# Kernel optimization log

Measured on AMD Instinct MI355X. Metric: run time of the kernel, lower is better.

Reference implementation:

```python
import jax, jax.numpy as jnp
import numpy as np

SHAPES = [(100, 100), (50, 50), (25, 25), (13, 13)]
N_HEADS, N_LEVELS, N_POINTS, D_MODEL, D_FFN = 8, 4, 4, 256, 1024
HEAD_DIM = D_MODEL // N_HEADS
S_TOTAL = sum(h * w for h, w in SHAPES)
BATCH = 2


def _layernorm(x, g, b, eps=1e-5):
    m = jnp.mean(x, -1, keepdims=True)
    v = jnp.mean((x - m) ** 2, -1, keepdims=True)
    return (x - m) * jax.lax.rsqrt(v + eps) * g + b


def _bilinear_sample(value_l, loc, Hl, Wl):
    # value_l: (N, Hl, Wl, nh, hd); loc: (N, Lq, nh, P, 2) normalized to [0,1]
    # Matches torch grid_sample(mode='bilinear', padding_mode='zeros', align_corners=False)
    x = loc[..., 0] * Wl - 0.5
    y = loc[..., 1] * Hl - 0.5
    x0 = jnp.floor(x); y0 = jnp.floor(y)
    wx1 = x - x0; wx0 = 1.0 - wx1
    wy1 = y - y0; wy0 = 1.0 - wy1
    x0i = x0.astype(jnp.int32); x1i = x0i + 1
    y0i = y0.astype(jnp.int32); y1i = y0i + 1
    N, Lq, nh, P = x.shape
    n_idx = jnp.arange(N)[:, None, None, None]
    h_idx = jnp.arange(nh)[None, None, :, None]

    def gather(yi, xi):
        valid = (yi >= 0) & (yi < Hl) & (xi >= 0) & (xi < Wl)
        yc = jnp.clip(yi, 0, Hl - 1); xc = jnp.clip(xi, 0, Wl - 1)
        v = value_l[n_idx, yc, xc, h_idx]  # (N, Lq, nh, P, hd)
        return v * valid[..., None].astype(v.dtype)

    return (gather(y0i, x0i) * (wy0 * wx0)[..., None]
            + gather(y0i, x1i) * (wy0 * wx1)[..., None]
            + gather(y1i, x0i) * (wy1 * wx0)[..., None]
            + gather(y1i, x1i) * (wy1 * wx1)[..., None])


def _forward(src, pos, reference_points, W_off, b_off, W_attn, b_attn, W_val, b_val,
             W_out, b_out, W1, b1, W2, b2, g1, beta1, g2, beta2):
    N, S, C = src.shape
    q = src + pos  # with_pos_embed
    # MSDeformAttn
    off = (q @ W_off + b_off).reshape(N, S, N_HEADS, N_LEVELS, N_POINTS, 2)
    aw = jax.nn.softmax((q @ W_attn + b_attn).reshape(N, S, N_HEADS, N_LEVELS * N_POINTS), axis=-1)
    aw = aw.reshape(N, S, N_HEADS, N_LEVELS, N_POINTS)
    value = (src @ W_val + b_val).reshape(N, S, N_HEADS, HEAD_DIM)
    # offset normalizer is (W_l, H_l) per level
    normalizer = jnp.array([[wl, hl] for hl, wl in SHAPES], dtype=src.dtype)  # (L, 2)
    loc = reference_points[:, :, None, :, None, :] + off / normalizer[None, None, None, :, None, :]
    out = jnp.zeros((N, S, N_HEADS, HEAD_DIM), src.dtype)
    start = 0
    for l, (Hl, Wl) in enumerate(SHAPES):
        v_l = value[:, start:start + Hl * Wl].reshape(N, Hl, Wl, N_HEADS, HEAD_DIM)
        sampled = _bilinear_sample(v_l, loc[:, :, :, l], Hl, Wl)  # (N,S,nh,P,hd)
        out = out + jnp.einsum('nqhp,nqhpd->nqhd', aw[:, :, :, l], sampled)
        start += Hl * Wl
    src2 = out.reshape(N, S, C) @ W_out + b_out
    # residual + norm1 (dropout is identity in eval)
    x = _layernorm(src + src2, g1, beta1)
    # FFN + residual + norm2
    ff = jax.nn.relu(x @ W1 + b1) @ W2 + b2
    return _layernorm(x + ff, g2, beta2)


def setup_inputs() -> dict:
    key = jax.random.key(0)
    ks = jax.random.split(key, 16)
    f32 = jnp.float32

    def w(k, shape, scale=0.02):
        return jax.random.normal(k, shape, dtype=f32) * scale

    return {
        "src": jax.random.normal(ks[0], (BATCH, S_TOTAL, D_MODEL), dtype=f32),
        "pos": jax.random.normal(ks[1], (BATCH, S_TOTAL, D_MODEL), dtype=f32),
        "reference_points": jax.random.uniform(ks[2], (BATCH, S_TOTAL, N_LEVELS, 2), dtype=f32),
        "spatial_shapes": jnp.array(SHAPES, dtype=jnp.int32),
        "level_start_index": jnp.array(np.cumsum([0] + [h * w for h, w in SHAPES[:-1]]), dtype=jnp.int32),
        "W_off": w(ks[3], (D_MODEL, N_HEADS * N_LEVELS * N_POINTS * 2)),
        "b_off": w(ks[4], (N_HEADS * N_LEVELS * N_POINTS * 2,), 0.5),
        "W_attn": w(ks[5], (D_MODEL, N_HEADS * N_LEVELS * N_POINTS)),
        "b_attn": w(ks[6], (N_HEADS * N_LEVELS * N_POINTS,)),
        "W_val": w(ks[7], (D_MODEL, D_MODEL)),
        "b_val": w(ks[8], (D_MODEL,)),
        "W_out": w(ks[9], (D_MODEL, D_MODEL)),
        "b_out": w(ks[10], (D_MODEL,)),
        "W1": w(ks[11], (D_MODEL, D_FFN)),
        "b1": w(ks[12], (D_FFN,)),
        "W2": w(ks[13], (D_FFN, D_MODEL)),
        "b2": w(ks[14], (D_MODEL,)),
        "g1": jnp.ones((D_MODEL,), f32),
        "beta1": jnp.zeros((D_MODEL,), f32),
        "g2": jnp.ones((D_MODEL,), f32),
        "beta2": jnp.zeros((D_MODEL,), f32),
    }


def reference(src, pos, reference_points, spatial_shapes, level_start_index,
              W_off, b_off, W_attn, b_attn, W_val, b_val, W_out, b_out,
              W1, b1, W2, b2, g1, beta1, g2, beta2):
    # spatial_shapes / level_start_index are static metadata mirrored by SHAPES
    return _forward(src, pos, reference_points, W_off, b_off, W_attn, b_attn,
                    W_val, b_val, W_out, b_out, W1, b1, W2, b2, g1, beta1, g2, beta2)
```

## Files before the change

### kernel.cpp

```cpp
#include <hip/hip_runtime.h>


typedef __bf16 bf16x8 __attribute__((ext_vector_type(8)));
typedef __bf16 bf16x4 __attribute__((ext_vector_type(4)));
typedef float floatx4 __attribute__((ext_vector_type(4)));

#define S_TOTAL 13294
#define M_ROWS  26588
#define M_PAD   26624
#define DMODEL  256

#define GLDS(g, l)                                                            \
    __builtin_amdgcn_global_load_lds(                                         \
        (const __attribute__((address_space(1))) void*)(g),                   \
        (__attribute__((address_space(3))) void*)(l), 16, 0, 0)

struct CvtArgs {
    const float *Woff, *Wattn, *Wval, *Wout, *W1, *W2, *boff, *battn;
};
__global__ __launch_bounds__(256) void cvt_all(CvtArgs a, __bf16* __restrict__ wdst,
                                               float* __restrict__ bc) {
    int i = blockIdx.x * 256 + threadIdx.x;
    if (i < 65536) {
        wdst[i] = (__bf16)a.Woff[(i & 255) * 256 + (i >> 8)];
    } else if (i < 98304) {
        int j = i - 65536;
        wdst[i] = (__bf16)a.Wattn[(j & 255) * 128 + (j >> 8)];
    } else if (i < 163840) {
        int j = i - 98304;
        wdst[i] = (__bf16)a.Wval[(j & 255) * 256 + (j >> 8)];
    } else if (i < 229376) {
        int j = i - 163840;
        wdst[i] = (__bf16)a.Wout[(j & 255) * 256 + (j >> 8)];
    } else if (i < 491520) {
        int j = i - 229376;
        wdst[i] = (__bf16)a.W1[(j & 255) * 1024 + (j >> 8)];
    } else if (i < 753664) {
        int j = i - 491520;
        wdst[i] = (__bf16)a.W2[(j & 1023) * 256 + (j >> 10)];
    } else if (i < 754048) {
        int j = i - 753664;
        bc[j] = (j < 256) ? a.boff[j] : a.battn[j - 256];
    }
}

__global__ __launch_bounds__(256) void prep_k(const float* __restrict__ src,
                                              const float* __restrict__ pos,
                                              __bf16* __restrict__ qb,
                                              __bf16* __restrict__ srcb) {
    int i4 = blockIdx.x * 256 + threadIdx.x;
    size_t e = (size_t)i4 * 4;
    if (e < (size_t)M_ROWS * DMODEL) {
        float4 s = *(const float4*)(src + e);
        float4 p = *(const float4*)(pos + e);
        bf16x4 q = {(__bf16)(s.x + p.x), (__bf16)(s.y + p.y),
                    (__bf16)(s.z + p.z), (__bf16)(s.w + p.w)};
        bf16x4 sb = {(__bf16)s.x, (__bf16)s.y, (__bf16)s.z, (__bf16)s.w};
        *(bf16x4*)(qb + e)   = q;
        *(bf16x4*)(srcb + e) = sb;
    } else {
        bf16x4 z = {(__bf16)0.f, (__bf16)0.f, (__bf16)0.f, (__bf16)0.f};
        *(bf16x4*)(qb + e)   = z;
        *(bf16x4*)(srcb + e) = z;
    }
}

template <bool RELU, bool BF16OUT, bool ACCUM>
__global__ __launch_bounds__(256, 2) void gemm128(const __bf16* __restrict__ A,
                                                  const __bf16* __restrict__ BT,
                                                  const float* __restrict__ bias,
                                                  float* __restrict__ Cf,
                                                  __bf16* __restrict__ Cb,
                                                  int N, int K, int ldb) {
    __shared__ __align__(16) char smem[20480];
    __bf16* As = (__bf16*)smem;
    __bf16* Bs = (__bf16*)(smem + 8192);
    const int tid  = threadIdx.x;
    const int bm   = blockIdx.y, bn = blockIdx.x;
    const int wave = tid >> 6, lane = tid & 63;
    const int wr   = wave >> 1, wc = wave & 1;
    const int l16  = lane & 15, quad = lane >> 4;

    floatx4 acc[4][4] = {};

    const int lr = tid >> 2;
    const int lc = (tid & 3) * 8;
    const __bf16* Ag0 = A  + (size_t)(bm * 128 + lr) * K + lc;
    const __bf16* Ag1 = Ag0 + (size_t)64 * K;
    const __bf16* Bg0 = BT + (size_t)(bn * 128 + lr) * ldb + lc;
    const __bf16* Bg1 = Bg0 + (size_t)64 * ldb;
    __bf16* Al0 = As + tid * 8;
    __bf16* Al1 = As + 64 * 32 + tid * 8;
    __bf16* Bl0 = Bs + tid * 8;
    __bf16* Bl1 = Bs + 64 * 32 + tid * 8;

    for (int k0 = 0; k0 < K; k0 += 32) {
        __syncthreads();
        GLDS(Ag0 + k0, Al0);
        GLDS(Ag1 + k0, Al1);
        GLDS(Bg0 + k0, Bl0);
        GLDS(Bg1 + k0, Bl1);
        __syncthreads();
        bf16x8 af[4], bfr[4];
#pragma unroll
        for (int i = 0; i < 4; i++)
            af[i] = *(const bf16x8*)(As + (wr * 64 + i * 16 + l16) * 32 + quad * 8);
#pragma unroll
        for (int j = 0; j < 4; j++)
            bfr[j] = *(const bf16x8*)(Bs + (wc * 64 + j * 16 + l16) * 32 + quad * 8);
#pragma unroll
        for (int i = 0; i < 4; i++)
#pragma unroll
            for (int j = 0; j < 4; j++)
                acc[i][j] = __builtin_amdgcn_mfma_f32_16x16x32_bf16(
                    af[i], bfr[j], acc[i][j], 0, 0, 0);
    }

    __syncthreads();
    float* patch = (float*)smem + wave * (64 * 20);
    const int row0 = bm * 128 + wr * 64;
    const int col0 = bn * 128 + wc * 64;
    const int plr = lane >> 2, plc = lane & 3;

#pragma unroll
    for (int j = 0; j < 4; j++) {
        int   n  = col0 + j * 16 + l16;
        float bv = bias ? bias[n] : 0.f;
#pragma unroll
        for (int i = 0; i < 4; i++)
#pragma unroll
            for (int r = 0; r < 4; r++) {
                float v = acc[i][j][r] + bv;
                if (RELU) v = fmaxf(v, 0.f);
                patch[(i * 16 + quad * 4 + r) * 20 + l16] = v;
            }
#pragma unroll
        for (int rr = 0; rr < 4; rr++) {
            int row = rr * 16 + plr;
            float4 v4 = *(float4*)&patch[row * 20 + plc * 4];
            size_t gi = (size_t)(row0 + row) * N + col0 + j * 16 + plc * 4;
            if (BF16OUT) {
                bf16x4 ob = {(__bf16)v4.x, (__bf16)v4.y, (__bf16)v4.z, (__bf16)v4.w};
                *(bf16x4*)(Cb + gi) = ob;
            } else if (ACCUM) {
                float4 c4 = *(const float4*)(Cf + gi);
                v4.x += c4.x; v4.y += c4.y; v4.z += c4.z; v4.w += c4.w;
                *(float4*)(Cf + gi) = v4;
            } else {
                *(float4*)(Cf + gi) = v4;
            }
        }
    }
}

__global__ __launch_bounds__(256) void sample_k(const float* __restrict__ offa,
                                                const __bf16* __restrict__ valb,
                                                const float* __restrict__ refp,
                                                __bf16* __restrict__ outb) {
    const int r   = blockIdx.x;
    const int tid = threadIdx.x;
    if (r >= M_ROWS) {
        outb[(size_t)r * 256 + tid] = (__bf16)0.f;
        return;
    }
    __shared__ float2 s_wo[128][4];
    const int n = (r >= S_TOTAL) ? 1 : 0;

    if (tid < 128) {
        const int HLc[4] = {100, 50, 25, 13};
        const int STc[4] = {0, 10000, 12500, 13125};
        int lp = tid & 15, l = lp >> 2;
        float logit = offa[(size_t)r * 384 + 256 + tid];
        float mx = logit;
        mx = fmaxf(mx, __shfl_xor(mx, 1));
        mx = fmaxf(mx, __shfl_xor(mx, 2));
        mx = fmaxf(mx, __shfl_xor(mx, 4));
        mx = fmaxf(mx, __shfl_xor(mx, 8));
        float e = __expf(logit - mx);
        float s = e;
        s += __shfl_xor(s, 1); s += __shfl_xor(s, 2);
        s += __shfl_xor(s, 4); s += __shfl_xor(s, 8);
        float aw = e / s;

        float2 o2 = *(const float2*)(offa + (size_t)r * 384 + tid * 2);
        float rx = refp[((size_t)r * 4 + l) * 2];
        float ry = refp[((size_t)r * 4 + l) * 2 + 1];
        int   Wl = HLc[l];
        float x = rx * (float)Wl + o2.x - 0.5f;
        float y = ry * (float)Wl + o2.y - 0.5f;
        float xf = floorf(x), yf = floorf(y);
        float wx1 = x - xf, wy1 = y - yf;
        float wx0 = 1.f - wx1, wy0 = 1.f - wy1;
        int x0 = (int)xf, y0 = (int)yf;
        int base = n * S_TOTAL + STc[l];
#pragma unroll
        for (int c = 0; c < 4; c++) {
            int yy = y0 + (c >> 1), xx = x0 + (c & 1);
            bool valid = (yy >= 0) & (yy < Wl) & (xx >= 0) & (xx < Wl);
            int yc = min(max(yy, 0), Wl - 1);
            int xc = min(max(xx, 0), Wl - 1);
            float w = ((c >> 1) ? wy1 : wy0) * ((c & 1) ? wx1 : wx0);
            int off = (base + yc * Wl + xc) * 512;
            s_wo[tid][c] = make_float2(valid ? w * aw : 0.f, __int_as_float(off));
        }
    }
    __syncthreads();

    const int h  = tid >> 5;
    const int pg = (tid >> 2) & 7;
    const int cg = tid & 3;
    const char* vbase = (const char*)valb + h * 64 + cg * 16;
    float a[8] = {};
#pragma unroll
    for (int pp = 0; pp < 2; pp++) {
        int idx = h * 16 + pg * 2 + pp;
#pragma unroll
        for (int c = 0; c < 4; c++) {
            float2 wo = s_wo[idx][c];
            float  w  = wo.x;
            bf16x8 v  = *(const bf16x8*)(vbase + __float_as_int(wo.y));
#pragma unroll
            for (int k = 0; k < 8; k++) a[k] += w * (float)v[k];
        }
    }
#pragma unroll
    for (int k = 0; k < 8; k++) {
        a[k] += __shfl_xor(a[k], 4);
        a[k] += __shfl_xor(a[k], 8);
        a[k] += __shfl_xor(a[k], 16);
    }
    if (pg == 0) {
        bf16x8 res;
#pragma unroll
        for (int k = 0; k < 8; k++) res[k] = (__bf16)a[k];
        *(bf16x8*)(outb + (size_t)r * 256 + h * 32 + cg * 8) = res;
    }
}

__global__ __launch_bounds__(64) void ln1_k(const float* __restrict__ src,
                                            const float* __restrict__ src2,
                                            const float* __restrict__ g,
                                            const float* __restrict__ b,
                                            float* __restrict__ x,
                                            __bf16* __restrict__ xb) {
    const int r = blockIdx.x, lane = threadIdx.x;
    if (r >= M_ROWS) {
        bf16x4 z = {(__bf16)0.f, (__bf16)0.f, (__bf16)0.f, (__bf16)0.f};
        *(bf16x4*)(xb + (size_t)r * 256 + lane * 4) = z;
        return;
    }
    size_t base = (size_t)r * 256 + lane * 4;
    float4 a = *(const float4*)(src + base);
    float4 c = *(const float4*)(src2 + base);
    float v0 = a.x + c.x, v1 = a.y + c.y, v2 = a.z + c.z, v3 = a.w + c.w;
    float s  = v0 + v1 + v2 + v3;
    float sq = v0 * v0 + v1 * v1 + v2 * v2 + v3 * v3;
    for (int o = 32; o > 0; o >>= 1) {
        s  += __shfl_xor(s, o);
        sq += __shfl_xor(sq, o);
    }
    float mean = s * (1.f / 256.f);
    float var  = sq * (1.f / 256.f) - mean * mean;
    float rs   = rsqrtf(var + 1e-5f);
    float4 gg = *(const float4*)(g + lane * 4);
    float4 bb = *(const float4*)(b + lane * 4);
    float o0 = (v0 - mean) * rs * gg.x + bb.x;
    float o1 = (v1 - mean) * rs * gg.y + bb.y;
    float o2 = (v2 - mean) * rs * gg.z + bb.z;
    float o3 = (v3 - mean) * rs * gg.w + bb.w;
    *(float4*)(x + base) = make_float4(o0, o1, o2, o3);
    bf16x4 ob = {(__bf16)o0, (__bf16)o1, (__bf16)o2, (__bf16)o3};
    *(bf16x4*)(xb + base) = ob;
}

__global__ __launch_bounds__(64) void ln2_k(const float* __restrict__ t,
                                            const float* __restrict__ g,
                                            const float* __restrict__ b,
                                            float* __restrict__ out) {
    const int r = blockIdx.x, lane = threadIdx.x;
    size_t base = (size_t)r * 256 + lane * 4;
    float4 a = *(const float4*)(t + base);
    float v0 = a.x, v1 = a.y, v2 = a.z, v3 = a.w;
    float s  = v0 + v1 + v2 + v3;
    float sq = v0 * v0 + v1 * v1 + v2 * v2 + v3 * v3;
    for (int o = 32; o > 0; o >>= 1) {
        s  += __shfl_xor(s, o);
        sq += __shfl_xor(sq, o);
    }
    float mean = s * (1.f / 256.f);
    float var  = sq * (1.f / 256.f) - mean * mean;
    float rs   = rsqrtf(var + 1e-5f);
    float4 gg = *(const float4*)(g + lane * 4);
    float4 bb = *(const float4*)(b + lane * 4);
    float4 o4;
    o4.x = (v0 - mean) * rs * gg.x + bb.x;
    o4.y = (v1 - mean) * rs * gg.y + bb.y;
    o4.z = (v2 - mean) * rs * gg.z + bb.z;
    o4.w = (v3 - mean) * rs * gg.w + bb.w;
    *(float4*)(out + base) = o4;
}

extern "C" void kernel_launch(void* const* d_in, const int* in_sizes, int n_in,
                              void* d_out, int out_size, void* d_ws, size_t ws_size,
                              hipStream_t stream) {
    const float* src  = (const float*)d_in[0];
    const float* pos  = (const float*)d_in[1];
    const float* refp = (const float*)d_in[2];
    const float* W_off  = (const float*)d_in[5];
    const float* b_off  = (const float*)d_in[6];
    const float* W_attn = (const float*)d_in[7];
    const float* b_attn = (const float*)d_in[8];
    const float* W_val  = (const float*)d_in[9];
    const float* b_val  = (const float*)d_in[10];
    const float* W_out  = (const float*)d_in[11];
    const float* b_out  = (const float*)d_in[12];
    const float* W1     = (const float*)d_in[13];
    const float* b1     = (const float*)d_in[14];
    const float* W2     = (const float*)d_in[15];
    const float* b2     = (const float*)d_in[16];
    const float* g1     = (const float*)d_in[17];
    const float* beta1  = (const float*)d_in[18];
    const float* g2     = (const float*)d_in[19];
    const float* beta2  = (const float*)d_in[20];
    float* out = (float*)d_out;

    const size_t RB = (size_t)M_PAD * 256 * 2;
    const size_t RF = (size_t)M_PAD * 256 * 4;
    char* ws = (char*)d_ws;
    __bf16* qb   = (__bf16*)(ws);
    __bf16* srcb = (__bf16*)(ws + RB);
    float*  offa = (float*)(ws + 2 * RB);
    __bf16* valb = (__bf16*)(ws + 2 * RB + (size_t)M_PAD * 384 * 4);
    __bf16* outb = qb;
    float*  src2 = (float*)(ws + RB);
    float*  x    = (float*)(ws + RB + RF);
    __bf16* xb   = qb;
    __bf16* hbh  = (__bf16*)(ws + 2 * RB + (size_t)M_PAD * 384 * 4);
    char*   regW = ws + 2 * RB + (size_t)M_PAD * 384 * 4 + (size_t)M_PAD * 512 * 2;

    __bf16* WTcomb = (__bf16*)regW;
    __bf16* WTval  = (__bf16*)(regW + 196608);
    __bf16* WTout  = (__bf16*)(regW + 327680);
    __bf16* WT1    = (__bf16*)(regW + 458752);
    __bf16* WT2    = (__bf16*)(regW + 983040);
    float*  bc     = (float*)(regW + 1507328);

    CvtArgs ca = {W_off, W_attn, W_val, W_out, W1, W2, b_off, b_attn};
    cvt_all<<<(754048 + 255) / 256, 256, 0, stream>>>(ca, WTcomb, bc);

    prep_k<<<M_PAD * 256 / 4 / 256, 256, 0, stream>>>(src, pos, qb, srcb);

    gemm128<false, false, false><<<dim3(3, M_PAD / 128), 256, 0, stream>>>(
        qb, WTcomb, bc, offa, nullptr, 384, 256, 256);
    gemm128<false, true, false><<<dim3(2, M_PAD / 128), 256, 0, stream>>>(
        srcb, WTval, b_val, nullptr, valb, 256, 256, 256);

    sample_k<<<M_PAD, 256, 0, stream>>>(offa, valb, refp, outb);

    gemm128<false, false, false><<<dim3(2, M_PAD / 128), 256, 0, stream>>>(
        outb, WTout, b_out, src2, nullptr, 256, 256, 256);
    ln1_k<<<M_PAD, 64, 0, stream>>>(src, src2, g1, beta1, x, xb);

    for (int half = 0; half < 2; half++) {
        gemm128<true, true, false><<<dim3(4, M_PAD / 128), 256, 0, stream>>>(
            xb, WT1 + (size_t)half * 512 * 256, b1 + half * 512, nullptr, hbh,
            512, 256, 256);
        gemm128<false, false, true><<<dim3(2, M_PAD / 128), 256, 0, stream>>>(
            hbh, WT2 + half * 512, half == 0 ? b2 : nullptr, x, nullptr,
            256, 512, 1024);
    }
    ln2_k<<<M_ROWS, 64, 0, stream>>>(x, g2, beta2, out);
}
```

Measured before the change: 345.1 us.

## Replace tiled GEMM with A-resident full-K GEMM reading B from global

Replaces the 128x128 k-loop GEMM with a kernel that loads the full-K A row panel (64 or 32 rows) into XOR-swizzled LDS once. Each of 8 waves then computes a slice of N with weights streamed directly from global/L2, with no per-k-step barriers. This removes the repeated syncthreads and the B staging through LDS, but relies on L2 caching for the small weight matrices. It also transposes the sampling kernel's shared weight/offset table to [corner][point] to change the LDS access pattern.

```diff
diff --git a/kernel.cpp b/kernel.cpp
--- a/kernel.cpp
+++ b/kernel.cpp
@@ -9,11 +9,6 @@
 #define M_ROWS  26588
 #define M_PAD   26624
 #define DMODEL  256
-
-#define GLDS(g, l)                                                            \
-    __builtin_amdgcn_global_load_lds(                                         \
-        (const __attribute__((address_space(1))) void*)(g),                   \
-        (__attribute__((address_space(3))) void*)(l), 16, 0, 0)
 
 struct CvtArgs {
     const float *Woff, *Wattn, *Wval, *Wout, *W1, *W2, *boff, *battn;
@@ -65,80 +60,76 @@
     }
 }
 
-template <bool RELU, bool BF16OUT, bool ACCUM>
-__global__ __launch_bounds__(256, 2) void gemm128(const __bf16* __restrict__ A,
-                                                  const __bf16* __restrict__ BT,
-                                                  const float* __restrict__ bias,
-                                                  float* __restrict__ Cf,
-                                                  __bf16* __restrict__ Cb,
-                                                  int N, int K, int ldb) {
-    __shared__ __align__(16) char smem[20480];
-    __bf16* As = (__bf16*)smem;
-    __bf16* Bs = (__bf16*)(smem + 8192);
+template <int BM, int KT, int J, bool RELU, bool BF16OUT, bool ACCUM>
+__global__ __launch_bounds__(512, 4) void gemm_ares(const __bf16* __restrict__ A,
+                                                    int lda,
+                                                    const __bf16* __restrict__ BT,
+                                                    int ldb,
+                                                    const float* __restrict__ bias,
+                                                    float* __restrict__ Cf,
+                                                    __bf16* __restrict__ Cb,
+                                                    int N) {
+    constexpr int GPR = KT / 8;
+    __shared__ __align__(16) __bf16 As[BM * KT];
+    __shared__ __align__(16) float  patch[8][16 * 20];
+
     const int tid  = threadIdx.x;
-    const int bm   = blockIdx.y, bn = blockIdx.x;
+    const int row0 = blockIdx.y * BM;
     const int wave = tid >> 6, lane = tid & 63;
-    const int wr   = wave >> 1, wc = wave & 1;
     const int l16  = lane & 15, quad = lane >> 4;
 
-    floatx4 acc[4][4] = {};
-
-    const int lr = tid >> 2;
-    const int lc = (tid & 3) * 8;
-    const __bf16* Ag0 = A  + (size_t)(bm * 128 + lr) * K + lc;
-    const __bf16* Ag1 = Ag0 + (size_t)64 * K;
-    const __bf16* Bg0 = BT + (size_t)(bn * 128 + lr) * ldb + lc;
-    const __bf16* Bg1 = Bg0 + (size_t)64 * ldb;
-    __bf16* Al0 = As + tid * 8;
-    __bf16* Al1 = As + 64 * 32 + tid * 8;
-    __bf16* Bl0 = Bs + tid * 8;
-    __bf16* Bl1 = Bs + 64 * 32 + tid * 8;
-
-    for (int k0 = 0; k0 < K; k0 += 32) {
-        __syncthreads();
-        GLDS(Ag0 + k0, Al0);
-        GLDS(Ag1 + k0, Al1);
-        GLDS(Bg0 + k0, Bl0);
-        GLDS(Bg1 + k0, Bl1);
-        __syncthreads();
-        bf16x8 af[4], bfr[4];
-#pragma unroll
-        for (int i = 0; i < 4; i++)
-            af[i] = *(const bf16x8*)(As + (wr * 64 + i * 16 + l16) * 32 + quad * 8);
-#pragma unroll
-        for (int j = 0; j < 4; j++)
-            bfr[j] = *(const bf16x8*)(Bs + (wc * 64 + j * 16 + l16) * 32 + quad * 8);
-#pragma unroll
-        for (int i = 0; i < 4; i++)
-#pragma unroll
-            for (int j = 0; j < 4; j++)
+#pragma unroll
+    for (int it = 0; it < BM * GPR / 512; it++) {
+        int fg = it * 512 + tid;
+        int m  = fg / GPR, g = fg % GPR;
+        bf16x8 v = *(const bf16x8*)(A + (size_t)(row0 + m) * lda + g * 8);
+        *(bf16x8*)(As + m * KT + (g ^ (m & 31)) * 8) = v;
+    }
+    __syncthreads();
+
+    const int n0 = blockIdx.x * (8 * J * 16) + wave * (J * 16);
+    floatx4 acc[BM / 16][J] = {};
+
+#pragma unroll 4
+    for (int ki = 0; ki < KT / 32; ki++) {
+        bf16x8 af[BM / 16], bfr[J];
+#pragma unroll
+        for (int i = 0; i < BM / 16; i++) {
+            int row = i * 16 + l16;
+            int g   = ki * 4 + quad;
+            af[i] = *(const bf16x8*)(As + row * KT + (g ^ (row & 31)) * 8);
+        }
+#pragma unroll
+        for (int j = 0; j < J; j++) {
+            int n = n0 + j * 16 + l16;
+            bfr[j] = *(const bf16x8*)(BT + (size_t)n * ldb + ki * 32 + quad * 8);
+        }
+#pragma unroll
+        for (int i = 0; i < BM / 16; i++)
+#pragma unroll
+            for (int j = 0; j < J; j++)
                 acc[i][j] = __builtin_amdgcn_mfma_f32_16x16x32_bf16(
                     af[i], bfr[j], acc[i][j], 0, 0, 0);
     }
 
-    __syncthreads();
-    float* patch = (float*)smem + wave * (64 * 20);
-    const int row0 = bm * 128 + wr * 64;
-    const int col0 = bn * 128 + wc * 64;
-    const int plr = lane >> 2, plc = lane & 3;
-
-#pragma unroll
-    for (int j = 0; j < 4; j++) {
-        int   n  = col0 + j * 16 + l16;
-        float bv = bias ? bias[n] : 0.f;
-#pragma unroll
-        for (int i = 0; i < 4; i++)
+    float bvj[J];
+#pragma unroll
+    for (int j = 0; j < J; j++) bvj[j] = bias ? bias[n0 + j * 16 + l16] : 0.f;
+
+    float* pat = patch[wave];
+    const int prow = lane >> 2, pc = lane & 3;
+#pragma unroll
+    for (int i = 0; i < BM / 16; i++)
+#pragma unroll
+        for (int j = 0; j < J; j++) {
 #pragma unroll
             for (int r = 0; r < 4; r++) {
-                float v = acc[i][j][r] + bv;
+                float v = acc[i][j][r] + bvj[j];
                 if (RELU) v = fmaxf(v, 0.f);
-                patch[(i * 16 + quad * 4 + r) * 20 + l16] = v;
+                pat[(quad * 4 + r) * 20 + l16] = v;
             }
-#pragma unroll
-        for (int rr = 0; rr < 4; rr++) {
-            int row = rr * 16 + plr;
-            float4 v4 = *(float4*)&patch[row * 20 + plc * 4];
-            size_t gi = (size_t)(row0 + row) * N + col0 + j * 16 + plc * 4;
+            float4 v4 = *(float4*)&pat[prow * 20 + pc * 4];
+            size_t gi = (size_t)(row0 + i * 16 + prow) * N + n0 + j * 16 + pc * 4;
             if (BF16OUT) {
                 bf16x4 ob = {(__bf16)v4.x, (__bf16)v4.y, (__bf16)v4.z, (__bf16)v4.w};
                 *(bf16x4*)(Cb + gi) = ob;
@@ -150,7 +141,6 @@
                 *(float4*)(Cf + gi) = v4;
             }
         }
-    }
 }
 
 __global__ __launch_bounds__(256) void sample_k(const float* __restrict__ offa,
@@ -163,7 +153,7 @@
         outb[(size_t)r * 256 + tid] = (__bf16)0.f;
         return;
     }
-    __shared__ float2 s_wo[128][4];
+    __shared__ float2 s_wo[4][128];
     const int n = (r >= S_TOTAL) ? 1 : 0;
 
     if (tid < 128) {
@@ -201,7 +191,7 @@
             int xc = min(max(xx, 0), Wl - 1);
             float w = ((c >> 1) ? wy1 : wy0) * ((c & 1) ? wx1 : wx0);
             int off = (base + yc * Wl + xc) * 512;
-            s_wo[tid][c] = make_float2(valid ? w * aw : 0.f, __int_as_float(off));
+            s_wo[c][tid] = make_float2(valid ? w * aw : 0.f, __int_as_float(off));
         }
     }
     __syncthreads();
@@ -216,7 +206,7 @@
         int idx = h * 16 + pg * 2 + pp;
 #pragma unroll
         for (int c = 0; c < 4; c++) {
-            float2 wo = s_wo[idx][c];
+            float2 wo = s_wo[c][idx];
             float  w  = wo.x;
             bf16x8 v  = *(const bf16x8*)(vbase + __float_as_int(wo.y));
 #pragma unroll
@@ -350,24 +340,24 @@
 
     prep_k<<<M_PAD * 256 / 4 / 256, 256, 0, stream>>>(src, pos, qb, srcb);
 
-    gemm128<false, false, false><<<dim3(3, M_PAD / 128), 256, 0, stream>>>(
-        qb, WTcomb, bc, offa, nullptr, 384, 256, 256);
-    gemm128<false, true, false><<<dim3(2, M_PAD / 128), 256, 0, stream>>>(
-        srcb, WTval, b_val, nullptr, valb, 256, 256, 256);
+    gemm_ares<64, 256, 3, false, false, false><<<dim3(1, 416), 512, 0, stream>>>(
+        qb, 256, WTcomb, 256, bc, offa, nullptr, 384);
+    gemm_ares<64, 256, 2, false, true, false><<<dim3(1, 416), 512, 0, stream>>>(
+        srcb, 256, WTval, 256, b_val, nullptr, valb, 256);
 
     sample_k<<<M_PAD, 256, 0, stream>>>(offa, valb, refp, outb);
 
-    gemm128<false, false, false><<<dim3(2, M_PAD / 128), 256, 0, stream>>>(
-        outb, WTout, b_out, src2, nullptr, 256, 256, 256);
+    gemm_ares<64, 256, 2, false, false, false><<<dim3(1, 416), 512, 0, stream>>>(
+        outb, 256, WTout, 256, b_out, src2, nullptr, 256);
     ln1_k<<<M_PAD, 64, 0, stream>>>(src, src2, g1, beta1, x, xb);
 
     for (int half = 0; half < 2; half++) {
-        gemm128<true, true, false><<<dim3(4, M_PAD / 128), 256, 0, stream>>>(
-            xb, WT1 + (size_t)half * 512 * 256, b1 + half * 512, nullptr, hbh,
-            512, 256, 256);
-        gemm128<false, false, true><<<dim3(2, M_PAD / 128), 256, 0, stream>>>(
-            hbh, WT2 + half * 512, half == 0 ? b2 : nullptr, x, nullptr,
-            256, 512, 1024);
+        gemm_ares<64, 256, 2, true, true, false><<<dim3(2, 416), 512, 0, stream>>>(
+            xb, 256, WT1 + (size_t)half * 512 * 256, 256, b1 + half * 512,
+            nullptr, hbh, 512);
+        gemm_ares<32, 512, 2, false, false, true><<<dim3(1, 832), 512, 0, stream>>>(
+            hbh, 512, WT2 + half * 512, 1024, half == 0 ? b2 : nullptr,
+            x, nullptr, 256);
     }
     ln2_k<<<M_ROWS, 64, 0, stream>>>(x, g2, beta2, out);
 }
```

Result: slower. 392.6 us (+13.8%).
